# Optimization experiments

Measured on AMD Instinct MI355X. Metric: run time of the kernel, lower is better.

## Reference

```python
import jax, jax.numpy as jnp
import numpy as np

B, S, D = 16, 2048, 256
K, CD = 8, 1024


def setup_inputs() -> dict:
    key = jax.random.key(0)
    k1, k2 = jax.random.split(key)
    x = jax.random.normal(k1, (B, S, D), dtype=jnp.float32)
    codebooks = jax.random.normal(k2, (K, CD, D), dtype=jnp.float32)
    return {"x": x, "codebooks": codebooks}


def _nearest(res, cb):
    # res: [N, d], cb: [cd_size, d]
    # squared L2 distance (same argmin as torch.cdist p=2)
    d2 = (jnp.sum(res * res, axis=1, keepdims=True)
          - 2.0 * res @ cb.T
          + jnp.sum(cb * cb, axis=1))  # [N, cd_size]
    enc = jnp.argmin(d2, axis=-1)      # [N]
    return enc, cb[enc]                # [N], [N, d]


def reference(x, codebooks):
    b, s, d = x.shape
    k = codebooks.shape[0]
    res = x.reshape(-1, d)             # running residual [N, d]
    quantised = jnp.zeros_like(res)
    loss_cd = jnp.float32(0.0)
    loss_enc = jnp.float32(0.0)
    encs = []
    sg = jax.lax.stop_gradient
    for i in range(k):
        enc, near = _nearest(res, codebooks[i])
        loss_cd = loss_cd + jnp.mean((sg(res) - near) ** 2)
        loss_enc = loss_enc + jnp.mean((res - sg(near)) ** 2)
        res = res - near
        quantised = quantised + near
        encs.append(enc)
    discrete_enc = jnp.stack(encs, axis=-1).reshape(b, s, k).astype(jnp.int64)
    # straight-through: forward value = sum of codebook vectors,
    # gradient flows through the final residual (as in the torch code)
    quantised_vectors = (res + sg(quantised - res)).reshape(b, s, d)
    return (loss_cd, loss_enc, discrete_enc, quantised_vectors)
```

## Files before the change

### kernel.cpp

```cpp
#include <hip/hip_runtime.h>

#define DD    256
#define KST   8
#define CDN   1024
#define NROWS 32768
#define ROWS  64
#define AST   64

__device__ float cbT_buf[(size_t)KST * 128 * CDN * 2];

__device__ __forceinline__ bool better(float a, int ja, float b, int jb_) {
    return (a < b) || (a == b && ja < jb_);
}

template <typename F>
__device__ __forceinline__ float np_sumsq_256(F ld) {
    float Sv = 0.f;
#pragma unroll
    for (int blk = 0; blk < 2; ++blk) {
        const int o = blk * 128;
        float w[16];
#pragma unroll
        for (int l = 0; l < 16; ++l) {
            float v[8];
#pragma unroll
            for (int j = 0; j < 8; ++j) {
                float xv = ld(o + 16 * j + l);
                v[j] = __fmul_rn(xv, xv);
            }
            float a01 = __fadd_rn(v[0], v[1]);
            float a23 = __fadd_rn(v[2], v[3]);
            float a45 = __fadd_rn(v[4], v[5]);
            float a67 = __fadd_rn(v[6], v[7]);
            w[l] = __fadd_rn(__fadd_rn(a01, a23), __fadd_rn(a45, a67));
        }
        float t8[8];
#pragma unroll
        for (int l = 0; l < 8; ++l) t8[l] = __fadd_rn(w[l], w[l + 8]);
        float t4[4];
#pragma unroll
        for (int l = 0; l < 4; ++l) t4[l] = __fadd_rn(t8[l], t8[l + 4]);
        float t2_0 = __fadd_rn(t4[0], t4[2]);
        float t2_1 = __fadd_rn(t4[1], t4[3]);
        float bs = __fadd_rn(t2_0, t2_1);
        Sv = (blk == 0) ? bs : __fadd_rn(Sv, bs);
    }
    return Sv;
}

__global__ __launch_bounds__(256) void norms_kernel(const float* __restrict__ cb,
                                                    float* __restrict__ n32) {
    int j = blockIdx.x * 256 + threadIdx.x;
    const float* p = cb + (size_t)j * DD;
    n32[j] = np_sumsq_256([&](int i) { return p[i]; });
}

__global__ __launch_bounds__(256) void tr_kernel(const float* __restrict__ cb) {
    int idx = blockIdx.x * 256 + threadIdx.x;
    int j  = idx & 1023;
    int c2 = (idx >> 10) & 127;
    int s  = idx >> 17;
    float2 v = *(const float2*)(cb + ((size_t)(s * CDN + j) * DD) + c2 * 2);
    *(float2*)(cbT_buf + (size_t)idx * 2) = v;
}

__global__ __launch_bounds__(512, 2) void rvq_kernel(const float* __restrict__ x,
                                                     const float* __restrict__ cbs,
                                                     const float* __restrict__ n32,
                                                     float* __restrict__ out) {
    __shared__ __align__(16) float a_t[DD][AST];
    __shared__ float rowS[ROWS];
    __shared__ float bestS[ROWS];
    __shared__ int   bestI[ROWS];
    __shared__ float wred[8];

    const int tid  = threadIdx.x;
    const int base = blockIdx.x * ROWS;
    const int cg   = tid & 63;
    const int ty   = tid >> 6;
    const int row0 = ty * 8;
    const int urow = tid & 63;
    const int ug   = tid >> 6;

    for (int i = tid; i < ROWS * DD / 4; i += 512) {
        int row = i >> 6;
        int dq  = i & 63;
        float4 v = ((const float4*)(x + (size_t)(base + row) * DD))[dq];
        int d = dq * 4;
        a_t[d + 0][row] = v.x; a_t[d + 1][row] = v.y;
        a_t[d + 2][row] = v.z; a_t[d + 3][row] = v.w;
    }

    float loss_acc = 0.f;

    for (int s = 0; s < KST; ++s) {
        const float* cb  = cbs + (size_t)s * CDN * DD;
        const float* nr  = n32 + s * CDN;
        const float* cts = cbT_buf + ((size_t)s << 18);
        __syncthreads();

        if (cg < 8) {
            int row = row0 + cg;
            rowS[row] = np_sumsq_256([&](int i) { return a_t[i][row]; });
            bestS[row] = 3.4e38f;
            bestI[row] = 0x7ffffff;
        }

        for (int h = 0; h < 2; ++h) {
            float acc[8][8];
#pragma unroll
            for (int sl = 0; sl < 8; ++sl)
#pragma unroll
                for (int r = 0; r < 8; ++r) acc[sl][r] = 0.f;

            const float* bp = cts + ((size_t)(h * 512) + cg) * 2;

            float2 bA_[8], bB_[8];
            float  xaR[8], yaR[8];

            auto LOADB = [&](float2* dst, int c) {
                const float* q = bp + (size_t)c * 2048;
#pragma unroll
                for (int sl = 0; sl < 8; ++sl)
                    dst[sl] = *(const float2*)(q + sl * 128);
            };
            auto LOADA = [&](float* dst, int kk) {
                float4 p0 = *(const float4*)&a_t[kk][row0];
                float4 p1 = *(const float4*)&a_t[kk][row0 + 4];
                dst[0] = p0.x; dst[1] = p0.y; dst[2] = p0.z; dst[3] = p0.w;
                dst[4] = p1.x; dst[5] = p1.y; dst[6] = p1.z; dst[7] = p1.w;
            };
            auto FMAX = [&](const float2* b, const float* a) {
#pragma unroll
                for (int sl = 0; sl < 8; ++sl)
#pragma unroll
                    for (int r = 0; r < 8; ++r)
                        acc[sl][r] = __builtin_fmaf(b[sl].x, a[r], acc[sl][r]);
            };
            auto FMAY = [&](const float2* b, const float* a) {
#pragma unroll
                for (int sl = 0; sl < 8; ++sl)
#pragma unroll
                    for (int r = 0; r < 8; ++r)
                        acc[sl][r] = __builtin_fmaf(b[sl].y, a[r], acc[sl][r]);
            };

            LOADB(bA_, 0);
            LOADA(xaR, 0);
#pragma unroll 1
            for (int c2 = 0; c2 < 128; c2 += 2) {
                LOADA(yaR, 2 * c2 + 1);
                LOADB(bB_, c2 + 1);
                FMAX(bA_, xaR);
                LOADA(xaR, 2 * c2 + 2);
                FMAY(bA_, yaR);
                LOADA(yaR, 2 * c2 + 3);
                {
                    int cn = (c2 + 2 < 128) ? (c2 + 2) : 127;
                    LOADB(bA_, cn);
                }
                FMAX(bB_, xaR);
                {
                    int kn = (2 * c2 + 4 < 256) ? (2 * c2 + 4) : 254;
                    LOADA(xaR, kn);
                }
                FMAY(bB_, yaR);
            }

            float nrv[8];
#pragma unroll
            for (int sl = 0; sl < 8; ++sl) nrv[sl] = nr[h * 512 + sl * 64 + cg];
#pragma unroll
            for (int r = 0; r < 8; ++r) {
                int row = row0 + r;
                float Sr = rowS[row];
                float t1 = 3.4e38f; int u1 = 0x7ffffff;
#pragma unroll
                for (int sl = 0; sl < 8; ++sl) {
                    int j = h * 512 + sl * 64 + cg;
                    float m2 = __fmul_rn(2.f, acc[sl][r]);
                    float sc2 = __fadd_rn(__fsub_rn(Sr, m2), nrv[sl]);
                    if (better(sc2, j, t1, u1)) { t1 = sc2; u1 = j; }
                }
#pragma unroll
                for (int off = 32; off >= 1; off >>= 1) {
                    float ob = __shfl_xor(t1, off, 64);
                    int   oj = __shfl_xor(u1, off, 64);
                    if (better(ob, oj, t1, u1)) { t1 = ob; u1 = oj; }
                }
                if (cg == r) {
                    if (better(t1, u1, bestS[row], bestI[row])) {
                        bestS[row] = t1; bestI[row] = u1;
                    }
                }
            }
        }

        if (cg < 8) {
            int row = row0 + cg;
            out[2 + (size_t)(base + row) * KST + s] = (float)bestI[row];
        }
        __syncthreads();

        {
            int bi = bestI[urow];
            const float4* cp = (const float4*)(cb + (size_t)bi * DD + ug * 32);
#pragma unroll
            for (int dq = 0; dq < 8; ++dq) {
                float4 v = cp[dq];
                int d = ug * 32 + dq * 4;
                float e0 = __fsub_rn(a_t[d + 0][urow], v.x); a_t[d + 0][urow] = e0;
                float e1 = __fsub_rn(a_t[d + 1][urow], v.y); a_t[d + 1][urow] = e1;
                float e2 = __fsub_rn(a_t[d + 2][urow], v.z); a_t[d + 2][urow] = e2;
                float e3 = __fsub_rn(a_t[d + 3][urow], v.w); a_t[d + 3][urow] = e3;
                loss_acc += e0 * e0 + e1 * e1 + e2 * e2 + e3 * e3;
            }
        }
    }
    __syncthreads();

    float* q = out + 2 + (size_t)NROWS * KST;
    for (int i = tid; i < ROWS * DD / 4; i += 512) {
        int row = i >> 6, dq = i & 63, d = dq * 4;
        float4 xv = ((const float4*)(x + (size_t)(base + row) * DD))[dq];
        float4 o;
        o.x = xv.x - a_t[d + 0][row];
        o.y = xv.y - a_t[d + 1][row];
        o.z = xv.z - a_t[d + 2][row];
        o.w = xv.w - a_t[d + 3][row];
        ((float4*)(q + (size_t)(base + row) * DD))[dq] = o;
    }
#pragma unroll
    for (int off = 32; off >= 1; off >>= 1) loss_acc += __shfl_down(loss_acc, off, 64);
    if ((tid & 63) == 0) wred[tid >> 6] = loss_acc;
    __syncthreads();
    if (tid == 0) {
        float t = ((wred[0] + wred[1]) + (wred[2] + wred[3]))
                + ((wred[4] + wred[5]) + (wred[6] + wred[7]));
        t *= (1.f / ((float)NROWS * (float)DD));
        atomicAdd(out + 0, t);
        atomicAdd(out + 1, t);
    }
}

extern "C" void kernel_launch(void* const* d_in, const int* in_sizes, int n_in,
                              void* d_out, int out_size, void* d_ws, size_t ws_size,
                              hipStream_t stream) {
    const float* x   = (const float*)d_in[0];
    const float* cbs = (const float*)d_in[1];
    float* out = (float*)d_out;
    float* n32 = (float*)d_ws;

    hipMemsetAsync(d_out, 0, 2 * sizeof(float), stream);
    tr_kernel<<<4096, 256, 0, stream>>>(cbs);
    norms_kernel<<<32, 256, 0, stream>>>(cbs, n32);
    rvq_kernel<<<NROWS / ROWS, 512, 0, stream>>>(x, cbs, n32, out);
}
```

Before: 2.180 ms.

## Stage codebook tiles in double-buffered LDS and broadcast activations via readlane

Codebook operands are no longer read per thread straight from global memory. Each block now cooperatively loads 8-k-pair tiles into a double-buffered shared-memory array, prefetching the next tile into registers while the current one is consumed. Activation values are read once per 64 k-steps into registers and broadcast across lanes with readlane, and the a_t stride is padded to 65 to avoid bank conflicts. The thread-to-codeword mapping becomes contiguous (cg*8+sl). In exchange the kernel adds 64KB of LDS, which likely cuts occupancy below the 2 blocks per CU it targets, and adds a block-wide barrier every tile.

```diff
diff --git a/kernel.cpp b/kernel.cpp
--- a/kernel.cpp
+++ b/kernel.cpp
@@ -5,7 +5,7 @@
 #define CDN   1024
 #define NROWS 32768
 #define ROWS  64
-#define AST   64
+#define AST   65
 
 __device__ float cbT_buf[(size_t)KST * 128 * CDN * 2];
 
@@ -69,6 +69,7 @@
                                                      const float* __restrict__ n32,
                                                      float* __restrict__ out) {
     __shared__ __align__(16) float a_t[DD][AST];
+    __shared__ __align__(16) float Bl[2][8][512][2];
     __shared__ float rowS[ROWS];
     __shared__ float bestS[ROWS];
     __shared__ int   bestI[ROWS];
@@ -92,6 +93,8 @@
     }
 
     float loss_acc = 0.f;
+    const int hi8 = tid >> 8;
+    const int rem = tid & 255;
 
     for (int s = 0; s < KST; ++s) {
         const float* cb  = cbs + (size_t)s * CDN * DD;
@@ -107,69 +110,77 @@
         }
 
         for (int h = 0; h < 2; ++h) {
+            __syncthreads();
+
+            float4 stg[4];
+#pragma unroll
+            for (int i = 0; i < 4; ++i) {
+                int kp = hi8 + 2 * i;
+                stg[i] = *(const float4*)(cts + (size_t)kp * 2048 + h * 1024 + rem * 4);
+            }
+#pragma unroll
+            for (int i = 0; i < 4; ++i)
+                ((float4*)&Bl[0][0][0][0])[tid + i * 512] = stg[i];
+
+            int cur = 0;
             float acc[8][8];
 #pragma unroll
             for (int sl = 0; sl < 8; ++sl)
 #pragma unroll
                 for (int r = 0; r < 8; ++r) acc[sl][r] = 0.f;
-
-            const float* bp = cts + ((size_t)(h * 512) + cg) * 2;
-
-            float2 bA_[8], bB_[8];
-            float  xaR[8], yaR[8];
-
-            auto LOADB = [&](float2* dst, int c) {
-                const float* q = bp + (size_t)c * 2048;
-#pragma unroll
-                for (int sl = 0; sl < 8; ++sl)
-                    dst[sl] = *(const float2*)(q + sl * 128);
-            };
-            auto LOADA = [&](float* dst, int kk) {
-                float4 p0 = *(const float4*)&a_t[kk][row0];
-                float4 p1 = *(const float4*)&a_t[kk][row0 + 4];
-                dst[0] = p0.x; dst[1] = p0.y; dst[2] = p0.z; dst[3] = p0.w;
-                dst[4] = p1.x; dst[5] = p1.y; dst[6] = p1.z; dst[7] = p1.w;
-            };
-            auto FMAX = [&](const float2* b, const float* a) {
-#pragma unroll
-                for (int sl = 0; sl < 8; ++sl)
+            float aQ[8];
+
+#pragma unroll 1
+            for (int t = 0; t < 16; ++t) {
+                __syncthreads();
+                if ((t & 3) == 0) {
+                    int q = t >> 2;
 #pragma unroll
                     for (int r = 0; r < 8; ++r)
-                        acc[sl][r] = __builtin_fmaf(b[sl].x, a[r], acc[sl][r]);
-            };
-            auto FMAY = [&](const float2* b, const float* a) {
-#pragma unroll
-                for (int sl = 0; sl < 8; ++sl)
-#pragma unroll
-                    for (int r = 0; r < 8; ++r)
-                        acc[sl][r] = __builtin_fmaf(b[sl].y, a[r], acc[sl][r]);
-            };
-
-            LOADB(bA_, 0);
-            LOADA(xaR, 0);
-#pragma unroll 1
-            for (int c2 = 0; c2 < 128; c2 += 2) {
-                LOADA(yaR, 2 * c2 + 1);
-                LOADB(bB_, c2 + 1);
-                FMAX(bA_, xaR);
-                LOADA(xaR, 2 * c2 + 2);
-                FMAY(bA_, yaR);
-                LOADA(yaR, 2 * c2 + 3);
-                {
-                    int cn = (c2 + 2 < 128) ? (c2 + 2) : 127;
-                    LOADB(bA_, cn);
-                }
-                FMAX(bB_, xaR);
-                {
-                    int kn = (2 * c2 + 4 < 256) ? (2 * c2 + 4) : 254;
-                    LOADA(xaR, kn);
-                }
-                FMAY(bB_, yaR);
-            }
-
-            float nrv[8];
-#pragma unroll
-            for (int sl = 0; sl < 8; ++sl) nrv[sl] = nr[h * 512 + sl * 64 + cg];
+                        aQ[r] = a_t[q * 64 + cg][row0 + r];
+                }
+                if (t < 15) {
+#pragma unroll
+                    for (int i = 0; i < 4; ++i) {
+                        int kp = hi8 + 2 * i;
+                        stg[i] = *(const float4*)(cts + (size_t)((t + 1) * 8 + kp) * 2048
+                                                      + h * 1024 + rem * 4);
+                    }
+                }
+#pragma unroll
+                for (int kp = 0; kp < 8; ++kp) {
+                    const float4* bp4 = (const float4*)&Bl[cur][kp][cg * 8][0];
+                    float4 b0 = bp4[0], b1 = bp4[1], b2 = bp4[2], b3 = bp4[3];
+                    float bk0[8] = {b0.x, b0.z, b1.x, b1.z, b2.x, b2.z, b3.x, b3.z};
+                    float bk1[8] = {b0.y, b0.w, b1.y, b1.w, b2.y, b2.w, b3.y, b3.w};
+#pragma unroll
+                    for (int kk = 0; kk < 2; ++kk) {
+                        int ln = (t & 3) * 16 + kp * 2 + kk;
+                        float ar[8];
+#pragma unroll
+                        for (int r = 0; r < 8; ++r)
+                            ar[r] = __int_as_float(
+                                __builtin_amdgcn_readlane(__float_as_int(aQ[r]), ln));
+                        const float* bsel = kk ? bk1 : bk0;
+#pragma unroll
+                        for (int sl = 0; sl < 8; ++sl)
+#pragma unroll
+                            for (int r = 0; r < 8; ++r)
+                                acc[sl][r] = __builtin_fmaf(bsel[sl], ar[r], acc[sl][r]);
+                    }
+                }
+                if (t < 15) {
+#pragma unroll
+                    for (int i = 0; i < 4; ++i)
+                        ((float4*)&Bl[cur ^ 1][0][0][0])[tid + i * 512] = stg[i];
+                }
+                cur ^= 1;
+            }
+
+            const float* nrp = nr + h * 512 + cg * 8;
+            float4 nA = *(const float4*)nrp;
+            float4 nB = *(const float4*)(nrp + 4);
+            float nrv[8] = {nA.x, nA.y, nA.z, nA.w, nB.x, nB.y, nB.z, nB.w};
 #pragma unroll
             for (int r = 0; r < 8; ++r) {
                 int row = row0 + r;
@@ -177,7 +188,7 @@
                 float t1 = 3.4e38f; int u1 = 0x7ffffff;
 #pragma unroll
                 for (int sl = 0; sl < 8; ++sl) {
-                    int j = h * 512 + sl * 64 + cg;
+                    int j = h * 512 + cg * 8 + sl;
                     float m2 = __fmul_rn(2.f, acc[sl][r]);
                     float sc2 = __fadd_rn(__fsub_rn(Sr, m2), nrv[sl]);
                     if (better(sc2, j, t1, u1)) { t1 = sc2; u1 = j; }
```

Measured after the change: 3.242 ms. 48.7% more time.
